# Performance work log

Measured on AMD Instinct MI355X. Metric: run time of the kernel, lower is better.

Reference implementation:

```python
import jax, jax.numpy as jnp
import numpy as np

B, N, E = 2, 2048, 1024
H, D = 16, 64  # num_heads, head_dim
BASE = 10000.0
EPS = 1e-5


def _lrpe(x, offset=0):
    """xmixers Lrpe (lrpe_type=1): activation (silu) then rotary position embedding.
    x: [b, n, h, d] -> [b, n, h, d]"""
    x = jax.nn.silu(x)
    b, n, h, d = x.shape
    inv_freq = BASE ** (-(jnp.arange(d // 2, dtype=jnp.float32) * 2.0) / d)  # [d/2]
    pos = jnp.arange(n, dtype=jnp.float32) + offset
    ang = pos[:, None] * inv_freq[None, :]            # [n, d/2]
    cos = jnp.cos(ang)[None, :, None, :].astype(x.dtype)
    sin = jnp.sin(ang)[None, :, None, :].astype(x.dtype)
    x1, x2 = x[..., : d // 2], x[..., d // 2:]
    return jnp.concatenate([x1 * cos - x2 * sin, x1 * sin + x2 * cos], axis=-1)


def setup_inputs() -> dict:
    key = jax.random.key(0)
    ks = jax.random.split(key, 8)
    std = 0.02
    return {
        "x": jax.random.normal(ks[0], (B, N, E), dtype=jnp.float32),
        "Wq": jax.random.normal(ks[1], (E, E), dtype=jnp.float32) * std,
        "Wk": jax.random.normal(ks[2], (E, E), dtype=jnp.float32) * std,
        "Wv": jax.random.normal(ks[3], (E, E), dtype=jnp.float32) * std,
        "Wo": jax.random.normal(ks[4], (E, E), dtype=jnp.float32) * std,
        "Wg1": jax.random.normal(ks[5], (E, D), dtype=jnp.float32) * std,
        "Wg2": jax.random.normal(ks[6], (D, E), dtype=jnp.float32) * std,
        "gamma": jnp.ones((E,), dtype=jnp.float32),
        "beta": jnp.zeros((E,), dtype=jnp.float32),
    }


def reference(x, Wq, Wk, Wv, Wo, Wg1, Wg2, gamma, beta):
    b, n, e = x.shape
    q = (x @ Wq).reshape(b, n, H, D)
    k = (x @ Wk).reshape(b, n, H, D)
    v = (x @ Wv).reshape(b, n, H, D)

    q = _lrpe(q, offset=0)
    k = _lrpe(k, offset=0)

    # causal linear attention: (q k^T * tril) @ v, no softmax
    energy = jnp.einsum('bnhd,bmhd->bhnm', q, k)            # [b,h,n,n]
    mask = jnp.tril(jnp.ones((n, n), dtype=x.dtype))
    energy = energy * mask
    out = jnp.einsum('bhnm,bmhd->bnhd', energy, v).reshape(b, n, e)

    # output gate: sigmoid(Linear(Linear(x)))
    gate = jax.nn.sigmoid((x @ Wg1) @ Wg2)
    out = out * gate

    # layernorm over embed_dim
    mu = jnp.mean(out, axis=-1, keepdims=True)
    var = jnp.mean(jnp.square(out - mu), axis=-1, keepdims=True)
    out = (out - mu) * jax.lax.rsqrt(var + EPS) * gamma + beta

    return out @ Wo
```

## Files before the change

kernel.cpp:

```cpp
#include <hip/hip_runtime.h>
#include <hip/hip_bf16.h>
#include <math.h>

#define B_ 2
#define N_ 2048
#define E_ 1024
#define H_ 16
#define D_ 64
#define HALF_ 32
#define CK 64
#define NC (N_/CK)
#define BN (B_*N_)
#define TLD 72
#define EPS_ 1e-5f

using bf16x8  = __attribute__((ext_vector_type(8))) short;
using f32x4   = __attribute__((ext_vector_type(4))) float;
using short4v = __attribute__((ext_vector_type(4))) short;

__device__ __forceinline__ float sigmoid_(float v){ return 1.0f/(1.0f + __expf(-v)); }

__device__ __forceinline__ unsigned short f2bf(float f){
  unsigned u = __float_as_uint(f);
  unsigned r = (u + 0x7fffu + ((u>>16)&1u)) >> 16;
  return (unsigned short)r;
}
__device__ __forceinline__ float bf2f(unsigned short h){
  return __uint_as_float(((unsigned)h)<<16);
}

#define GLDS16(gp, lp) __builtin_amdgcn_global_load_lds( \
    (const __attribute__((address_space(1))) void*)(gp), \
    (__attribute__((address_space(3))) void*)(lp), 16, 0, 0)

__global__ __launch_bounds__(256) void sincos_kernel(float* __restrict__ ct,
                                                     float* __restrict__ st){
  int i = blockIdx.x*256 + threadIdx.x;
  int n = i >> 5, j = i & (HALF_-1);
  double invf = exp(((double)(-2*j)/(double)D_) * log(10000.0));
  double ang = (double)n * invf;
  ct[i] = (float)cos(ang);
  st[i] = (float)sin(ang);
}

__global__ __launch_bounds__(256) void xsplit_kernel(const float* __restrict__ x,
    short* __restrict__ xh, short* __restrict__ xl){
  int i = blockIdx.x*256 + threadIdx.x;
  float4 vv = ((const float4*)x)[i];
  float vs[4] = {vv.x, vv.y, vv.z, vv.w};
  short4v h, l;
  #pragma unroll
  for (int j=0;j<4;j++){
    unsigned short hb = f2bf(vs[j]);
    h[j] = (short)hb;
    l[j] = (short)f2bf(vs[j] - bf2f(hb));
  }
  ((short4v*)xh)[i] = h;
  ((short4v*)xl)[i] = l;
}

__global__ __launch_bounds__(256) void wsplit_kernel(const float* __restrict__ W,
    short* __restrict__ Wth, short* __restrict__ Wtl, int K, int N){
  __shared__ float T[64][65];
  int k0 = blockIdx.x*64, n0 = blockIdx.y*64;
  int tid = threadIdx.x;
  #pragma unroll
  for (int it=0; it<4; ++it){
    int idx = it*256 + tid;
    int r = idx >> 4, c = (idx & 15) << 2;
    float4 v = *(const float4*)&W[(size_t)(k0+r)*N + n0 + c];
    T[c+0][r]=v.x; T[c+1][r]=v.y; T[c+2][r]=v.z; T[c+3][r]=v.w;
  }
  __syncthreads();
  #pragma unroll
  for (int it=0; it<2; ++it){
    int idx = it*256 + tid;
    int r = idx >> 3, c8 = (idx & 7) << 3;
    bf16x8 h, l;
    #pragma unroll
    for (int j=0;j<8;j++){
      float v = T[r][c8+j];
      unsigned short hb = f2bf(v);
      h[j] = (short)hb;
      l[j] = (short)f2bf(v - bf2f(hb));
    }
    size_t o = (size_t)(n0+r)*K + k0 + c8;
    *(bf16x8*)&Wth[o] = h;
    *(bf16x8*)&Wtl[o] = l;
  }
}

template<int EPI>
__global__ __launch_bounds__(256) void gemm_mfma(
    const short* __restrict__ Ah, const short* __restrict__ Al,
    const short* __restrict__ Bh, const short* __restrict__ Bl,
    float* __restrict__ C, short* __restrict__ Ch, short* __restrict__ Cl,
    float* __restrict__ Cq, float* __restrict__ Ck,
    short* __restrict__ Cvh, short* __restrict__ Cvl,
    int M, int N, int K)
{
  __shared__ __align__(16) short sAh[128*64];
  __shared__ __align__(16) short sAl[128*64];
  __shared__ __align__(16) short sBh[64*64];
  __shared__ __align__(16) short sBl[64*64];
  const int tid = threadIdx.x;
  const int l = tid & 63, w = tid >> 6;
  const int wm = w >> 1, wn = w & 1;
  const int m0 = blockIdx.x*128, n0 = blockIdx.y*64;
  const int Kb = K*2;
  f32x4 acc[4][2] = {};

  const char* gAh = (const char*)Ah;
  const char* gAl = (const char*)Al;
  const char* gBh = (const char*)Bh;
  const char* gBl = (const char*)Bl;

  const int nkt = K/64;
  for (int kt = 0; kt < nkt; ++kt){
    const int kbyte = kt*128;
    #pragma unroll
    for (int i=0;i<4;i++){
      int p   = i*4096 + tid*16;
      int row = p >> 7;
      int c   = (p & 127) ^ ((row & 7) << 4);
      size_t go = (size_t)(m0+row)*Kb + kbyte + c;
      char* lb  = (char*)sAh + i*4096 + w*1024;
      char* lb2 = (char*)sAl + i*4096 + w*1024;
      GLDS16(gAh + go, lb);
      GLDS16(gAl + go, lb2);
    }
    #pragma unroll
    for (int i=0;i<2;i++){
      int p   = i*4096 + tid*16;
      int row = p >> 7;
      int c   = (p & 127) ^ ((row & 7) << 4);
      size_t go = (size_t)(n0+row)*Kb + kbyte + c;
      char* lb  = (char*)sBh + i*4096 + w*1024;
      char* lb2 = (char*)sBl + i*4096 + w*1024;
      GLDS16(gBh + go, lb);
      GLDS16(gBl + go, lb2);
    }
    __syncthreads();
    #pragma unroll
    for (int kb=0;kb<2;kb++){
      const int cb = kb*64 + (l>>4)*16;
      bf16x8 ah[4], al[4], bh2[2], bl2[2];
      #pragma unroll
      for (int mb=0;mb<4;mb++){
        int row = wm*64 + mb*16 + (l&15);
        int off = row*128 + (cb ^ ((row&7)<<4));
        ah[mb] = *(const bf16x8*)((const char*)sAh + off);
        al[mb] = *(const bf16x8*)((const char*)sAl + off);
      }
      #pragma unroll
      for (int nb=0;nb<2;nb++){
        int row = wn*32 + nb*16 + (l&15);
        int off = row*128 + (cb ^ ((row&7)<<4));
        bh2[nb] = *(const bf16x8*)((const char*)sBh + off);
        bl2[nb] = *(const bf16x8*)((const char*)sBl + off);
      }
      #pragma unroll
      for (int mb=0;mb<4;mb++)
        #pragma unroll
        for (int nb=0;nb<2;nb++){
          acc[mb][nb] = __builtin_amdgcn_mfma_f32_16x16x32_bf16(ah[mb], bh2[nb], acc[mb][nb], 0,0,0);
          acc[mb][nb] = __builtin_amdgcn_mfma_f32_16x16x32_bf16(ah[mb], bl2[nb], acc[mb][nb], 0,0,0);
          acc[mb][nb] = __builtin_amdgcn_mfma_f32_16x16x32_bf16(al[mb], bh2[nb], acc[mb][nb], 0,0,0);
        }
    }
    __syncthreads();
  }
  #pragma unroll
  for (int mb=0;mb<4;mb++)
    #pragma unroll
    for (int nb=0;nb<2;nb++)
      #pragma unroll
      for (int r=0;r<4;r++){
        int row = m0 + wm*64 + mb*16 + (l>>4)*4 + r;
        int colg = n0 + wn*32 + nb*16 + (l&15);
        float v = acc[mb][nb][r];
        if (EPI == 0){
          C[(size_t)row*N + colg] = v;
        } else if (EPI == 2){
          unsigned short hb = f2bf(v);
          Ch[(size_t)row*N + colg] = (short)hb;
          Cl[(size_t)row*N + colg] = (short)f2bf(v - bf2f(hb));
        } else if (EPI == 3){
          if (colg < 1024){
            Cq[(size_t)row*1024 + colg] = v * sigmoid_(v);
          } else if (colg < 2048){
            Ck[(size_t)row*1024 + colg - 1024] = v * sigmoid_(v);
          } else {
            unsigned short hb = f2bf(v);
            Cvh[(size_t)row*1024 + colg - 2048] = (short)hb;
            Cvl[(size_t)row*1024 + colg - 2048] = (short)f2bf(v - bf2f(hb));
          }
        }
      }
}

__global__ __launch_bounds__(256) void rope_kernel(
    const float* __restrict__ qf, const float* __restrict__ kf,
    const float* __restrict__ ct, const float* __restrict__ st,
    short* __restrict__ qh, short* __restrict__ ql,
    short* __restrict__ kh, short* __restrict__ kl)
{
  int i = blockIdx.x*256 + threadIdx.x;
  int j0 = (i & 7) << 2;
  int h  = (i >> 3) & (H_-1);
  int n  = (i >> 7) & (N_-1);
  int b  = i >> 18;
  size_t base = ((size_t)(b*N_ + n))*E_ + h*D_;
  float4 c4 = *(const float4*)(ct + n*HALF_ + j0);
  float4 s4 = *(const float4*)(st + n*HALF_ + j0);
  float cc[4] = {c4.x,c4.y,c4.z,c4.w};
  float ss[4] = {s4.x,s4.y,s4.z,s4.w};
  #pragma unroll
  for (int which=0; which<2; ++which){
    const float* src = which ? kf : qf;
    short* dh = which ? kh : qh;
    short* dl = which ? kl : ql;
    float4 x1 = *(const float4*)(src + base + j0);
    float4 x2 = *(const float4*)(src + base + HALF_ + j0);
    float a1[4] = {x1.x,x1.y,x1.z,x1.w};
    float a2[4] = {x2.x,x2.y,x2.z,x2.w};
    short4v o1h,o1l,o2h,o2l;
    #pragma unroll
    for (int j=0;j<4;j++){
      float r1 = a1[j]*cc[j] - a2[j]*ss[j];
      float r2 = a1[j]*ss[j] + a2[j]*cc[j];
      unsigned short h1 = f2bf(r1), h2 = f2bf(r2);
      o1h[j]=(short)h1; o1l[j]=(short)f2bf(r1 - bf2f(h1));
      o2h[j]=(short)h2; o2l[j]=(short)f2bf(r2 - bf2f(h2));
    }
    *(short4v*)(dh + base + j0) = o1h;
    *(short4v*)(dl + base + j0) = o1l;
    *(short4v*)(dh + base + HALF_ + j0) = o2h;
    *(short4v*)(dl + base + HALF_ + j0) = o2l;
  }
}

__global__ __launch_bounds__(256) void chunk_kv_kernel(
    const short* __restrict__ kh, const short* __restrict__ kl,
    const short* __restrict__ vh, const short* __restrict__ vl,
    float* __restrict__ kvbuf)
{
  __shared__ __align__(16) short sKth[64*TLD], sKtl[64*TLD];
  __shared__ __align__(16) short sVth[64*TLD], sVtl[64*TLD];
  int bid = blockIdx.x;
  int c = bid & (NC-1), bh = bid >> 5;
  int b = bh >> 4, h = bh & 15;
  int tid = threadIdx.x;
  const int l = tid & 63, w = tid >> 6;
  const size_t rb = ((size_t)(b*N_ + c*CK))*E_ + h*D_;
  #pragma unroll
  for (int it=0; it<4; ++it){
    int f = it*256 + tid;
    int m = f >> 4, d0 = (f & 15) << 2;
    short4v a  = *(const short4v*)(kh + rb + (size_t)m*E_ + d0);
    short4v b2 = *(const short4v*)(kl + rb + (size_t)m*E_ + d0);
    short4v cc = *(const short4v*)(vh + rb + (size_t)m*E_ + d0);
    short4v dd = *(const short4v*)(vl + rb + (size_t)m*E_ + d0);
    #pragma unroll
    for (int j=0;j<4;j++){
      sKth[(d0+j)*TLD + m] = a[j];
      sKtl[(d0+j)*TLD + m] = b2[j];
      sVth[(d0+j)*TLD + m] = cc[j];
      sVtl[(d0+j)*TLD + m] = dd[j];
    }
  }
  __syncthreads();
  f32x4 acc[4] = {};
  #pragma unroll
  for (int ks=0; ks<2; ++ks){
    int acb = ks*64 + (l>>4)*16;
    int arow = w*16 + (l&15);
    bf16x8 aH = *(const bf16x8*)((const char*)sKth + arow*(TLD*2) + acb);
    bf16x8 aL = *(const bf16x8*)((const char*)sKtl + arow*(TLD*2) + acb);
    #pragma unroll
    for (int db=0; db<4; ++db){
      int brow = db*16 + (l&15);
      bf16x8 bH = *(const bf16x8*)((const char*)sVth + brow*(TLD*2) + acb);
      bf16x8 bL = *(const bf16x8*)((const char*)sVtl + brow*(TLD*2) + acb);
      acc[db] = __builtin_amdgcn_mfma_f32_16x16x32_bf16(aH, bH, acc[db],0,0,0);
      acc[db] = __builtin_amdgcn_mfma_f32_16x16x32_bf16(aH, bL, acc[db],0,0,0);
      acc[db] = __builtin_amdgcn_mfma_f32_16x16x32_bf16(aL, bH, acc[db],0,0,0);
    }
  }
  float* outp = kvbuf + ((size_t)bh*NC + c)*D_*D_;
  #pragma unroll
  for (int db=0;db<4;db++)
    #pragma unroll
    for (int r=0;r<4;r++){
      int din = w*16 + (l>>4)*4 + r;
      int dout = db*16 + (l&15);
      outp[(size_t)din*D_ + dout] = acc[db][r];
    }
}

__global__ __launch_bounds__(256) void kv_scan_kernel(float* __restrict__ kvbuf){
  int bh = blockIdx.x >> 4, seg = blockIdx.x & 15;
  int e = seg*256 + threadIdx.x;
  float* base = kvbuf + (size_t)bh*NC*D_*D_ + e;
  float run = 0.f;
  #pragma unroll 4
  for (int c=0;c<NC;c++){
    float v = base[(size_t)c*D_*D_];
    base[(size_t)c*D_*D_] = run;
    run += v;
  }
}

__global__ __launch_bounds__(256) void attn_mfma_kernel(
    const short* __restrict__ qh, const short* __restrict__ ql,
    const short* __restrict__ kh, const short* __restrict__ kl,
    const short* __restrict__ vh, const short* __restrict__ vl,
    const float* __restrict__ kvbuf, float* __restrict__ attn)
{
  __shared__ __align__(16) short sQh[4096], sQl[4096];
  __shared__ __align__(16) short sKh[4096], sKl[4096];
  __shared__ __align__(16) short sVth[64*TLD], sVtl[64*TLD];
  __shared__ __align__(16) short sKVth[64*TLD], sKVtl[64*TLD];
  const int tid = threadIdx.x;
  const int l = tid & 63, w = tid >> 6;
  const int bid = blockIdx.x;
  const int c = bid & (NC-1), bh = bid >> 5;
  const int b = bh >> 4, h = bh & 15;
  const size_t rowbase = (size_t)(b*N_ + c*CK);

  #pragma unroll
  for (int p=0;p<2;p++){
    int base = p*4096 + w*1024;
    int db = base + l*16;
    int row = db >> 7, col = db & 127;
    size_t src = ((rowbase + row)*E_ + h*D_)*2 + (size_t)(col ^ ((row&7)<<4));
    GLDS16((const char*)qh + src, (char*)sQh + base);
    GLDS16((const char*)ql + src, (char*)sQl + base);
    GLDS16((const char*)kh + src, (char*)sKh + base);
    GLDS16((const char*)kl + src, (char*)sKl + base);
  }

  {
    const short* vhb = vh + rowbase*E_ + h*D_;
    const short* vlb = vl + rowbase*E_ + h*D_;
    const float* kvb = kvbuf + ((size_t)bh*NC + c)*D_*D_;
    #pragma unroll
    for (int it=0; it<4; ++it){
      int f = it*256 + tid;
      int m = f >> 4, d0 = (f & 15) << 2;
      short4v a  = *(const short4v*)(vhb + (size_t)m*E_ + d0);
      short4v b2 = *(const short4v*)(vlb + (size_t)m*E_ + d0);
      float4 kvv = *(const float4*)(kvb + m*D_ + d0);
      float kvs[4] = {kvv.x,kvv.y,kvv.z,kvv.w};
      #pragma unroll
      for (int j=0;j<4;j++){
        sVth[(d0+j)*TLD + m] = a[j];
        sVtl[(d0+j)*TLD + m] = b2[j];
        unsigned short hb = f2bf(kvs[j]);
        sKVth[(d0+j)*TLD + m] = (short)hb;
        sKVtl[(d0+j)*TLD + m] = (short)f2bf(kvs[j] - bf2f(hb));
      }
    }
  }
  __syncthreads();

  f32x4 sacc[4] = {};
  #pragma unroll
  for (int ks=0; ks<2; ++ks){
    int arow = w*16 + (l&15);
    int acb = ks*64 + (l>>4)*16;
    int aoff = arow*128 + (acb ^ ((arow&7)<<4));
    bf16x8 aH = *(const bf16x8*)((const char*)sQh + aoff);
    bf16x8 aL = *(const bf16x8*)((const char*)sQl + aoff);
    #pragma unroll
    for (int nb=0;nb<4;nb++){
      int brow = nb*16 + (l&15);
      int boff = brow*128 + (acb ^ ((brow&7)<<4));
      bf16x8 bH = *(const bf16x8*)((const char*)sKh + boff);
      bf16x8 bL = *(const bf16x8*)((const char*)sKl + boff);
      sacc[nb] = __builtin_amdgcn_mfma_f32_16x16x32_bf16(aH, bH, sacc[nb],0,0,0);
      sacc[nb] = __builtin_amdgcn_mfma_f32_16x16x32_bf16(aH, bL, sacc[nb],0,0,0);
      sacc[nb] = __builtin_amdgcn_mfma_f32_16x16x32_bf16(aL, bH, sacc[nb],0,0,0);
    }
  }
  __syncthreads();
  #pragma unroll
  for (int nb=0;nb<4;nb++)
    #pragma unroll
    for (int r=0;r<4;r++){
      int n = w*16 + (l>>4)*4 + r;
      int m = nb*16 + (l&15);
      float sv = (m <= n) ? sacc[nb][r] : 0.0f;
      unsigned short hb = f2bf(sv);
      int off = n*128 + ((2*m) ^ ((n&7)<<4));
      *(short*)((char*)sKh + off) = (short)hb;
      *(short*)((char*)sKl + off) = (short)f2bf(sv - bf2f(hb));
    }
  __syncthreads();

  f32x4 oacc[4] = {};
  #pragma unroll
  for (int ks=0; ks<2; ++ks){
    int arow = w*16 + (l&15);
    int acb = ks*64 + (l>>4)*16;
    int aoff = arow*128 + (acb ^ ((arow&7)<<4));
    bf16x8 sH = *(const bf16x8*)((const char*)sKh + aoff);
    bf16x8 sL = *(const bf16x8*)((const char*)sKl + aoff);
    bf16x8 qH = *(const bf16x8*)((const char*)sQh + aoff);
    bf16x8 qL = *(const bf16x8*)((const char*)sQl + aoff);
    #pragma unroll
    for (int db=0; db<4; ++db){
      int brow = db*16 + (l&15);
      bf16x8 vH  = *(const bf16x8*)((const char*)sVth  + brow*(TLD*2) + acb);
      bf16x8 vL  = *(const bf16x8*)((const char*)sVtl  + brow*(TLD*2) + acb);
      bf16x8 kvH = *(const bf16x8*)((const char*)sKVth + brow*(TLD*2) + acb);
      bf16x8 kvL = *(const bf16x8*)((const char*)sKVtl + brow*(TLD*2) + acb);
      oacc[db] = __builtin_amdgcn_mfma_f32_16x16x32_bf16(sH, vH,  oacc[db],0,0,0);
      oacc[db] = __builtin_amdgcn_mfma_f32_16x16x32_bf16(sH, vL,  oacc[db],0,0,0);
      oacc[db] = __builtin_amdgcn_mfma_f32_16x16x32_bf16(sL, vH,  oacc[db],0,0,0);
      oacc[db] = __builtin_amdgcn_mfma_f32_16x16x32_bf16(qH, kvH, oacc[db],0,0,0);
      oacc[db] = __builtin_amdgcn_mfma_f32_16x16x32_bf16(qH, kvL, oacc[db],0,0,0);
      oacc[db] = __builtin_amdgcn_mfma_f32_16x16x32_bf16(qL, kvH, oacc[db],0,0,0);
    }
  }
  float* ob = attn + rowbase*E_ + h*D_;
  #pragma unroll
  for (int db=0;db<4;db++)
    #pragma unroll
    for (int r=0;r<4;r++){
      int n = w*16 + (l>>4)*4 + r;
      int d = db*16 + (l&15);
      ob[(size_t)n*E_ + d] = oacc[db][r];
    }
}

__global__ __launch_bounds__(256) void gate_ln_kernel(const float* __restrict__ attn,
    const float* __restrict__ g2,
    const float* __restrict__ gamma, const float* __restrict__ beta,
    short* __restrict__ yh, short* __restrict__ yl)
{
  __shared__ float red[8];
  __shared__ float stats[2];
  int r = blockIdx.x, tid = threadIdx.x;
  float vals[4]; float s=0.f, sq=0.f;
  #pragma unroll
  for (int i=0;i<4;i++){
    int e = i*256 + tid;
    float a = attn[(size_t)r*E_ + e];
    float g = g2[(size_t)r*E_ + e];
    float val = a * sigmoid_(g);
    vals[i] = val; s += val; sq += val*val;
  }
  #pragma unroll
  for (int off=32; off>=1; off>>=1){
    s  += __shfl_down(s,  off, 64);
    sq += __shfl_down(sq, off, 64);
  }
  int lane = tid & 63, wid = tid >> 6;
  if (lane == 0){ red[wid] = s; red[4+wid] = sq; }
  __syncthreads();
  if (tid == 0){
    float ts = red[0]+red[1]+red[2]+red[3];
    float tq = red[4]+red[5]+red[6]+red[7];
    float mu = ts / (float)E_;
    float var = tq / (float)E_ - mu*mu;
    stats[0] = mu; stats[1] = rsqrtf(var + EPS_);
  }
  __syncthreads();
  float mu = stats[0], rs = stats[1];
  #pragma unroll
  for (int i=0;i<4;i++){
    int e = i*256 + tid;
    float yv = (vals[i]-mu)*rs*gamma[e] + beta[e];
    unsigned short hb = f2bf(yv);
    yh[(size_t)r*E_ + e] = (short)hb;
    yl[(size_t)r*E_ + e] = (short)f2bf(yv - bf2f(hb));
  }
}

extern "C" void kernel_launch(void* const* d_in, const int* in_sizes, int n_in,
                              void* d_out, int out_size, void* d_ws, size_t ws_size,
                              hipStream_t stream) {
  const float* x    = (const float*)d_in[0];
  const float* Wq   = (const float*)d_in[1];
  const float* Wk   = (const float*)d_in[2];
  const float* Wv   = (const float*)d_in[3];
  const float* Wo   = (const float*)d_in[4];
  const float* Wg1  = (const float*)d_in[5];
  const float* Wg2  = (const float*)d_in[6];
  const float* gamma= (const float*)d_in[7];
  const float* beta = (const float*)d_in[8];
  float* out = (float*)d_out;

  char* ws = (char*)d_ws;
  const size_t MB = 1024*1024;
  float* qf    = (float*)(ws + 0*MB);
  float* kf    = (float*)(ws + 16*MB);
  short* xh    = (short*)(ws + 32*MB);
  short* xl    = (short*)(ws + 40*MB);
  short* vh    = (short*)(ws + 48*MB);
  short* vl    = (short*)(ws + 56*MB);
  short* qhb   = (short*)(ws + 64*MB);
  short* qlb   = (short*)(ws + 72*MB);
  short* khb   = (short*)(ws + 80*MB);
  short* klb   = (short*)(ws + 88*MB);
  float* kv    = (float*)(ws + 96*MB);
  short* wqkvh = (short*)(ws + 112*MB);
  short* wqkvl = (short*)(ws + 118*MB);
  short* woh   = (short*)(ws + 124*MB);
  short* wol   = (short*)(ws + 126*MB);
  float* ct    = (float*)(ws + 128*MB);
  float* st    = (float*)(ws + 128*MB + 256*1024);
  short* g1h   = (short*)(ws + 129*MB);
  short* g1l   = (short*)(ws + 129*MB + 512*1024);
  short* wg1h  = (short*)(ws + 130*MB);
  short* wg1l  = (short*)(ws + 130*MB + 128*1024);
  short* wg2h  = (short*)(ws + 130*MB + 256*1024);
  short* wg2l  = (short*)(ws + 130*MB + 384*1024);
  float* g2    = qf;
  float* attnb = kf;
  short* yh    = xh;
  short* yl    = xl;

  dim3 blk(256);
  sincos_kernel<<<dim3(N_*HALF_/256), blk, 0, stream>>>(ct, st);
  xsplit_kernel<<<dim3(BN*E_/4/256), blk, 0, stream>>>(x, xh, xl);
  wsplit_kernel<<<dim3(16,16), blk, 0, stream>>>(Wq, wqkvh,               wqkvl,               E_, E_);
  wsplit_kernel<<<dim3(16,16), blk, 0, stream>>>(Wk, wqkvh + 1024*1024,   wqkvl + 1024*1024,   E_, E_);
  wsplit_kernel<<<dim3(16,16), blk, 0, stream>>>(Wv, wqkvh + 2048*1024,   wqkvl + 2048*1024,   E_, E_);
  wsplit_kernel<<<dim3(16,16), blk, 0, stream>>>(Wo, woh, wol, E_, E_);
  wsplit_kernel<<<dim3(16,1),  blk, 0, stream>>>(Wg1, wg1h, wg1l, E_, D_);
  wsplit_kernel<<<dim3(1,16),  blk, 0, stream>>>(Wg2, wg2h, wg2l, D_, E_);

  gemm_mfma<3><<<dim3(BN/128, 3072/64), blk, 0, stream>>>(
      xh, xl, wqkvh, wqkvl, nullptr, nullptr, nullptr, qf, kf, vh, vl, BN, 3072, E_);
  gemm_mfma<2><<<dim3(BN/128, 1), blk, 0, stream>>>(
      xh, xl, wg1h, wg1l, nullptr, g1h, g1l, nullptr, nullptr, nullptr, nullptr, BN, D_, E_);
  rope_kernel<<<dim3(BN*H_*8/256), blk, 0, stream>>>(qf, kf, ct, st, qhb, qlb, khb, klb);
  gemm_mfma<0><<<dim3(BN/128, E_/64), blk, 0, stream>>>(
      g1h, g1l, wg2h, wg2l, g2, nullptr, nullptr, nullptr, nullptr, nullptr, nullptr, BN, E_, D_);
  chunk_kv_kernel<<<dim3(B_*H_*NC), blk, 0, stream>>>(khb, klb, vh, vl, kv);
  kv_scan_kernel<<<dim3(B_*H_*16), blk, 0, stream>>>(kv);
  attn_mfma_kernel<<<dim3(B_*H_*NC), blk, 0, stream>>>(qhb, qlb, khb, klb, vh, vl, kv, attnb);
  gate_ln_kernel<<<dim3(BN), blk, 0, stream>>>(attnb, g2, gamma, beta, yh, yl);
  gemm_mfma<0><<<dim3(BN/128, E_/64), blk, 0, stream>>>(
      yh, yl, woh, wol, out, nullptr, nullptr, nullptr, nullptr, nullptr, nullptr, BN, E_, E_);
}
```

Before: 299.3 us.

## Fuse SiLU+RoPE into QKV GEMM epilogue, merge gate GEMM, widen tiles

The QKV projection GEMM now applies SiLU, rotary embedding and the bf16 hi/lo split directly in its epilogue, so the separate rope kernel and the fp32 q/k intermediates are no longer written and re-read. The first gate projection (Wg1) is appended as extra columns of the same GEMM, padded with zeros up to 3200, which removes one launch. GEMM tiles grow from 128x64 to 128x128, with launch bounds asking for 2 blocks per CU. In exchange there are more registers and LDS per block, some wasted work on the zero padding, and reduced block counts for the smaller GEMMs.

```diff
diff --git a/kernel.cpp b/kernel.cpp
--- a/kernel.cpp
+++ b/kernel.cpp
@@ -13,6 +13,7 @@
 #define BN (B_*N_)
 #define TLD 72
 #define EPS_ 1e-5f
+#define NQKV 3200
 
 using bf16x8  = __attribute__((ext_vector_type(8))) short;
 using f32x4   = __attribute__((ext_vector_type(4))) float;
@@ -59,6 +60,14 @@
   ((short4v*)xl)[i] = l;
 }
 
+__global__ __launch_bounds__(256) void zfill_kernel(short* __restrict__ a,
+                                                    short* __restrict__ b){
+  int i = blockIdx.x*256 + threadIdx.x;
+  short4v z = {0,0,0,0};
+  ((short4v*)a)[i] = z;
+  ((short4v*)b)[i] = z;
+}
+
 __global__ __launch_bounds__(256) void wsplit_kernel(const float* __restrict__ W,
     short* __restrict__ Wth, short* __restrict__ Wtl, int K, int N){
   __shared__ float T[64][65];
@@ -91,24 +100,27 @@
 }
 
 template<int EPI>
-__global__ __launch_bounds__(256) void gemm_mfma(
+__global__ __launch_bounds__(256,2) void gemm_mfma(
     const short* __restrict__ Ah, const short* __restrict__ Al,
     const short* __restrict__ Bh, const short* __restrict__ Bl,
-    float* __restrict__ C, short* __restrict__ Ch, short* __restrict__ Cl,
-    float* __restrict__ Cq, float* __restrict__ Ck,
-    short* __restrict__ Cvh, short* __restrict__ Cvl,
+    float* __restrict__ C,
+    short* __restrict__ Qh, short* __restrict__ Ql,
+    short* __restrict__ Kh, short* __restrict__ Kl,
+    short* __restrict__ Vh, short* __restrict__ Vl,
+    short* __restrict__ G1h, short* __restrict__ G1l,
+    const float* __restrict__ ct, const float* __restrict__ st,
     int M, int N, int K)
 {
   __shared__ __align__(16) short sAh[128*64];
   __shared__ __align__(16) short sAl[128*64];
-  __shared__ __align__(16) short sBh[64*64];
-  __shared__ __align__(16) short sBl[64*64];
+  __shared__ __align__(16) short sBh[128*64];
+  __shared__ __align__(16) short sBl[128*64];
   const int tid = threadIdx.x;
   const int l = tid & 63, w = tid >> 6;
   const int wm = w >> 1, wn = w & 1;
-  const int m0 = blockIdx.x*128, n0 = blockIdx.y*64;
+  const int m0 = blockIdx.x*128, n0 = blockIdx.y*128;
   const int Kb = K*2;
-  f32x4 acc[4][2] = {};
+  f32x4 acc[4][4] = {};
 
   const char* gAh = (const char*)Ah;
   const char* gAl = (const char*)Al;
@@ -123,28 +135,20 @@
       int p   = i*4096 + tid*16;
       int row = p >> 7;
       int c   = (p & 127) ^ ((row & 7) << 4);
-      size_t go = (size_t)(m0+row)*Kb + kbyte + c;
-      char* lb  = (char*)sAh + i*4096 + w*1024;
-      char* lb2 = (char*)sAl + i*4096 + w*1024;
-      GLDS16(gAh + go, lb);
-      GLDS16(gAl + go, lb2);
-    }
-    #pragma unroll
-    for (int i=0;i<2;i++){
-      int p   = i*4096 + tid*16;
-      int row = p >> 7;
-      int c   = (p & 127) ^ ((row & 7) << 4);
-      size_t go = (size_t)(n0+row)*Kb + kbyte + c;
-      char* lb  = (char*)sBh + i*4096 + w*1024;
-      char* lb2 = (char*)sBl + i*4096 + w*1024;
-      GLDS16(gBh + go, lb);
-      GLDS16(gBl + go, lb2);
+      size_t goA = (size_t)(m0+row)*Kb + kbyte + c;
+      size_t goB = (size_t)(n0+row)*Kb + kbyte + c;
+      char* lbase = (char*)nullptr;
+      (void)lbase;
+      GLDS16(gAh + goA, (char*)sAh + i*4096 + w*1024);
+      GLDS16(gAl + goA, (char*)sAl + i*4096 + w*1024);
+      GLDS16(gBh + goB, (char*)sBh + i*4096 + w*1024);
+      GLDS16(gBl + goB, (char*)sBl + i*4096 + w*1024);
     }
     __syncthreads();
     #pragma unroll
     for (int kb=0;kb<2;kb++){
       const int cb = kb*64 + (l>>4)*16;
-      bf16x8 ah[4], al[4], bh2[2], bl2[2];
+      bf16x8 ah[4], al[4], bh2[4], bl2[4];
       #pragma unroll
       for (int mb=0;mb<4;mb++){
         int row = wm*64 + mb*16 + (l&15);
@@ -153,8 +157,8 @@
         al[mb] = *(const bf16x8*)((const char*)sAl + off);
       }
       #pragma unroll
-      for (int nb=0;nb<2;nb++){
-        int row = wn*32 + nb*16 + (l&15);
+      for (int nb=0;nb<4;nb++){
+        int row = wn*64 + nb*16 + (l&15);
         int off = row*128 + (cb ^ ((row&7)<<4));
         bh2[nb] = *(const bf16x8*)((const char*)sBh + off);
         bl2[nb] = *(const bf16x8*)((const char*)sBl + off);
@@ -162,7 +166,7 @@
       #pragma unroll
       for (int mb=0;mb<4;mb++)
         #pragma unroll
-        for (int nb=0;nb<2;nb++){
+        for (int nb=0;nb<4;nb++){
           acc[mb][nb] = __builtin_amdgcn_mfma_f32_16x16x32_bf16(ah[mb], bh2[nb], acc[mb][nb], 0,0,0);
           acc[mb][nb] = __builtin_amdgcn_mfma_f32_16x16x32_bf16(ah[mb], bl2[nb], acc[mb][nb], 0,0,0);
           acc[mb][nb] = __builtin_amdgcn_mfma_f32_16x16x32_bf16(al[mb], bh2[nb], acc[mb][nb], 0,0,0);
@@ -170,73 +174,77 @@
     }
     __syncthreads();
   }
-  #pragma unroll
-  for (int mb=0;mb<4;mb++)
-    #pragma unroll
-    for (int nb=0;nb<2;nb++)
-      #pragma unroll
-      for (int r=0;r<4;r++){
-        int row = m0 + wm*64 + mb*16 + (l>>4)*4 + r;
-        int colg = n0 + wn*32 + nb*16 + (l&15);
-        float v = acc[mb][nb][r];
-        if (EPI == 0){
-          C[(size_t)row*N + colg] = v;
-        } else if (EPI == 2){
-          unsigned short hb = f2bf(v);
-          Ch[(size_t)row*N + colg] = (short)hb;
-          Cl[(size_t)row*N + colg] = (short)f2bf(v - bf2f(hb));
-        } else if (EPI == 3){
-          if (colg < 1024){
-            Cq[(size_t)row*1024 + colg] = v * sigmoid_(v);
-          } else if (colg < 2048){
-            Ck[(size_t)row*1024 + colg - 1024] = v * sigmoid_(v);
-          } else {
+
+  if (EPI == 0){
+    #pragma unroll
+    for (int mb=0;mb<4;mb++)
+      #pragma unroll
+      for (int nb=0;nb<4;nb++)
+        #pragma unroll
+        for (int r=0;r<4;r++){
+          int row = m0 + wm*64 + mb*16 + (l>>4)*4 + r;
+          int colg = n0 + wn*64 + nb*16 + (l&15);
+          C[(size_t)row*N + colg] = acc[mb][nb][r];
+        }
+  } else {
+    const int colg0 = n0 + wn*64;
+    if (colg0 < 2048){
+      short* dh = (colg0 < 1024) ? Qh : Kh;
+      short* dl = (colg0 < 1024) ? Ql : Kl;
+      const int ebase = colg0 & 1023;
+      #pragma unroll
+      for (int mb=0;mb<4;mb++)
+        #pragma unroll
+        for (int nbp=0;nbp<2;nbp++)
+          #pragma unroll
+          for (int r=0;r<4;r++){
+            int row = m0 + wm*64 + mb*16 + (l>>4)*4 + r;
+            int d1 = nbp*16 + (l&15);
+            float a1 = acc[mb][nbp][r];
+            float a2 = acc[mb][nbp+2][r];
+            float x1 = a1 * sigmoid_(a1);
+            float x2 = a2 * sigmoid_(a2);
+            int n = row & (N_-1);
+            float cv = ct[n*HALF_ + d1];
+            float sv = st[n*HALF_ + d1];
+            float r1 = x1*cv - x2*sv;
+            float r2 = x1*sv + x2*cv;
+            size_t o1 = (size_t)row*E_ + ebase + d1;
+            size_t o2 = o1 + HALF_;
+            unsigned short h1 = f2bf(r1);
+            dh[o1] = (short)h1; dl[o1] = (short)f2bf(r1 - bf2f(h1));
+            unsigned short h2 = f2bf(r2);
+            dh[o2] = (short)h2; dl[o2] = (short)f2bf(r2 - bf2f(h2));
+          }
+    } else if (colg0 < 3072){
+      #pragma unroll
+      for (int mb=0;mb<4;mb++)
+        #pragma unroll
+        for (int nb=0;nb<4;nb++)
+          #pragma unroll
+          for (int r=0;r<4;r++){
+            int row = m0 + wm*64 + mb*16 + (l>>4)*4 + r;
+            int e = colg0 - 2048 + nb*16 + (l&15);
+            float v = acc[mb][nb][r];
             unsigned short hb = f2bf(v);
-            Cvh[(size_t)row*1024 + colg - 2048] = (short)hb;
-            Cvl[(size_t)row*1024 + colg - 2048] = (short)f2bf(v - bf2f(hb));
+            Vh[(size_t)row*E_ + e] = (short)hb;
+            Vl[(size_t)row*E_ + e] = (short)f2bf(v - bf2f(hb));
           }
-        }
-      }
-}
-
-__global__ __launch_bounds__(256) void rope_kernel(
-    const float* __restrict__ qf, const float* __restrict__ kf,
-    const float* __restrict__ ct, const float* __restrict__ st,
-    short* __restrict__ qh, short* __restrict__ ql,
-    short* __restrict__ kh, short* __restrict__ kl)
-{
-  int i = blockIdx.x*256 + threadIdx.x;
-  int j0 = (i & 7) << 2;
-  int h  = (i >> 3) & (H_-1);
-  int n  = (i >> 7) & (N_-1);
-  int b  = i >> 18;
-  size_t base = ((size_t)(b*N_ + n))*E_ + h*D_;
-  float4 c4 = *(const float4*)(ct + n*HALF_ + j0);
-  float4 s4 = *(const float4*)(st + n*HALF_ + j0);
-  float cc[4] = {c4.x,c4.y,c4.z,c4.w};
-  float ss[4] = {s4.x,s4.y,s4.z,s4.w};
-  #pragma unroll
-  for (int which=0; which<2; ++which){
-    const float* src = which ? kf : qf;
-    short* dh = which ? kh : qh;
-    short* dl = which ? kl : ql;
-    float4 x1 = *(const float4*)(src + base + j0);
-    float4 x2 = *(const float4*)(src + base + HALF_ + j0);
-    float a1[4] = {x1.x,x1.y,x1.z,x1.w};
-    float a2[4] = {x2.x,x2.y,x2.z,x2.w};
-    short4v o1h,o1l,o2h,o2l;
-    #pragma unroll
-    for (int j=0;j<4;j++){
-      float r1 = a1[j]*cc[j] - a2[j]*ss[j];
-      float r2 = a1[j]*ss[j] + a2[j]*cc[j];
-      unsigned short h1 = f2bf(r1), h2 = f2bf(r2);
-      o1h[j]=(short)h1; o1l[j]=(short)f2bf(r1 - bf2f(h1));
-      o2h[j]=(short)h2; o2l[j]=(short)f2bf(r2 - bf2f(h2));
-    }
-    *(short4v*)(dh + base + j0) = o1h;
-    *(short4v*)(dl + base + j0) = o1l;
-    *(short4v*)(dh + base + HALF_ + j0) = o2h;
-    *(short4v*)(dl + base + HALF_ + j0) = o2l;
+    } else if (colg0 < 3136){
+      #pragma unroll
+      for (int mb=0;mb<4;mb++)
+        #pragma unroll
+        for (int nb=0;nb<4;nb++)
+          #pragma unroll
+          for (int r=0;r<4;r++){
+            int row = m0 + wm*64 + mb*16 + (l>>4)*4 + r;
+            int e = nb*16 + (l&15);
+            float v = acc[mb][nb][r];
+            unsigned short hb = f2bf(v);
+            G1h[(size_t)row*D_ + e] = (short)hb;
+            G1l[(size_t)row*D_ + e] = (short)f2bf(v - bf2f(hb));
+          }
+    }
   }
 }
 
@@ -494,8 +502,8 @@
 
   char* ws = (char*)d_ws;
   const size_t MB = 1024*1024;
-  float* qf    = (float*)(ws + 0*MB);
-  float* kf    = (float*)(ws + 16*MB);
+  float* g2    = (float*)(ws + 0*MB);
+  float* attnb = (float*)(ws + 16*MB);
   short* xh    = (short*)(ws + 32*MB);
   short* xl    = (short*)(ws + 40*MB);
   short* vh    = (short*)(ws + 48*MB);
@@ -504,45 +512,44 @@
   short* qlb   = (short*)(ws + 72*MB);
   short* khb   = (short*)(ws + 80*MB);
   short* klb   = (short*)(ws + 88*MB);
+  short* g1h   = (short*)(ws + 96*MB);
+  short* g1l   = (short*)(ws + 96*MB + 512*1024);
   float* kv    = (float*)(ws + 96*MB);
   short* wqkvh = (short*)(ws + 112*MB);
-  short* wqkvl = (short*)(ws + 118*MB);
-  short* woh   = (short*)(ws + 124*MB);
-  short* wol   = (short*)(ws + 126*MB);
-  float* ct    = (float*)(ws + 128*MB);
-  float* st    = (float*)(ws + 128*MB + 256*1024);
-  short* g1h   = (short*)(ws + 129*MB);
-  short* g1l   = (short*)(ws + 129*MB + 512*1024);
-  short* wg1h  = (short*)(ws + 130*MB);
-  short* wg1l  = (short*)(ws + 130*MB + 128*1024);
-  short* wg2h  = (short*)(ws + 130*MB + 256*1024);
-  short* wg2l  = (short*)(ws + 130*MB + 384*1024);
-  float* g2    = qf;
-  float* attnb = kf;
+  short* wqkvl = (short*)(ws + 119*MB);
+  short* woh   = (short*)(ws + 126*MB);
+  short* wol   = (short*)(ws + 128*MB);
+  short* wg2h  = (short*)(ws + 130*MB);
+  short* wg2l  = (short*)(ws + 130*MB + 128*1024);
+  float* ct    = (float*)(ws + 130*MB + 256*1024);
+  float* st    = (float*)(ws + 130*MB + 512*1024);
   short* yh    = xh;
   short* yl    = xl;
 
   dim3 blk(256);
   sincos_kernel<<<dim3(N_*HALF_/256), blk, 0, stream>>>(ct, st);
   xsplit_kernel<<<dim3(BN*E_/4/256), blk, 0, stream>>>(x, xh, xl);
-  wsplit_kernel<<<dim3(16,16), blk, 0, stream>>>(Wq, wqkvh,               wqkvl,               E_, E_);
-  wsplit_kernel<<<dim3(16,16), blk, 0, stream>>>(Wk, wqkvh + 1024*1024,   wqkvl + 1024*1024,   E_, E_);
-  wsplit_kernel<<<dim3(16,16), blk, 0, stream>>>(Wv, wqkvh + 2048*1024,   wqkvl + 2048*1024,   E_, E_);
+  wsplit_kernel<<<dim3(16,16), blk, 0, stream>>>(Wq, wqkvh,             wqkvl,             E_, E_);
+  wsplit_kernel<<<dim3(16,16), blk, 0, stream>>>(Wk, wqkvh + 1024*1024, wqkvl + 1024*1024, E_, E_);
+  wsplit_kernel<<<dim3(16,16), blk, 0, stream>>>(Wv, wqkvh + 2048*1024, wqkvl + 2048*1024, E_, E_);
+  wsplit_kernel<<<dim3(16,1),  blk, 0, stream>>>(Wg1, wqkvh + 3072*1024, wqkvl + 3072*1024, E_, D_);
+  zfill_kernel<<<dim3(64), blk, 0, stream>>>(wqkvh + 3136*1024, wqkvl + 3136*1024);
   wsplit_kernel<<<dim3(16,16), blk, 0, stream>>>(Wo, woh, wol, E_, E_);
-  wsplit_kernel<<<dim3(16,1),  blk, 0, stream>>>(Wg1, wg1h, wg1l, E_, D_);
   wsplit_kernel<<<dim3(1,16),  blk, 0, stream>>>(Wg2, wg2h, wg2l, D_, E_);
 
-  gemm_mfma<3><<<dim3(BN/128, 3072/64), blk, 0, stream>>>(
-      xh, xl, wqkvh, wqkvl, nullptr, nullptr, nullptr, qf, kf, vh, vl, BN, 3072, E_);
-  gemm_mfma<2><<<dim3(BN/128, 1), blk, 0, stream>>>(
-      xh, xl, wg1h, wg1l, nullptr, g1h, g1l, nullptr, nullptr, nullptr, nullptr, BN, D_, E_);
-  rope_kernel<<<dim3(BN*H_*8/256), blk, 0, stream>>>(qf, kf, ct, st, qhb, qlb, khb, klb);
-  gemm_mfma<0><<<dim3(BN/128, E_/64), blk, 0, stream>>>(
-      g1h, g1l, wg2h, wg2l, g2, nullptr, nullptr, nullptr, nullptr, nullptr, nullptr, BN, E_, D_);
+  gemm_mfma<3><<<dim3(BN/128, NQKV/128), blk, 0, stream>>>(
+      xh, xl, wqkvh, wqkvl, nullptr,
+      qhb, qlb, khb, klb, vh, vl, g1h, g1l, ct, st, BN, NQKV, E_);
+  gemm_mfma<0><<<dim3(BN/128, E_/128), blk, 0, stream>>>(
+      g1h, g1l, wg2h, wg2l, g2,
+      nullptr,nullptr,nullptr,nullptr,nullptr,nullptr,nullptr,nullptr,
+      nullptr, nullptr, BN, E_, D_);
   chunk_kv_kernel<<<dim3(B_*H_*NC), blk, 0, stream>>>(khb, klb, vh, vl, kv);
   kv_scan_kernel<<<dim3(B_*H_*16), blk, 0, stream>>>(kv);
   attn_mfma_kernel<<<dim3(B_*H_*NC), blk, 0, stream>>>(qhb, qlb, khb, klb, vh, vl, kv, attnb);
   gate_ln_kernel<<<dim3(BN), blk, 0, stream>>>(attnb, g2, gamma, beta, yh, yl);
-  gemm_mfma<0><<<dim3(BN/128, E_/64), blk, 0, stream>>>(
-      yh, yl, woh, wol, out, nullptr, nullptr, nullptr, nullptr, nullptr, nullptr, BN, E_, E_);
-}
+  gemm_mfma<0><<<dim3(BN/128, E_/128), blk, 0, stream>>>(
+      yh, yl, woh, wol, out,
+      nullptr,nullptr,nullptr,nullptr,nullptr,nullptr,nullptr,nullptr,
+      nullptr, nullptr, BN, E_, E_);
+}
```

Measured after the change: 274.8 us. 8.2% less time.
